# Kernel optimization log

Measured on AMD Instinct MI355X. Metric: run time of the kernel, lower is better.

The kernel has to match this reference:

```python
import jax, jax.numpy as jnp
import numpy as np

B, I, H, O, E, K = 1024, 512, 2048, 512, 8, 2


def setup_inputs() -> dict:
    key = jax.random.key(0)
    k = jax.random.split(key, 7)
    s = 0.02
    return {
        "x": jax.random.normal(k[0], (B, I), dtype=jnp.float32),
        "Wg": jax.random.normal(k[1], (I, E), dtype=jnp.float32) * s,
        "bg": jnp.zeros((E,), dtype=jnp.float32),
        "W1": jax.random.normal(k[2], (E, I, H), dtype=jnp.float32) * s,
        "b1": jnp.zeros((E, H), dtype=jnp.float32),
        "W2": jax.random.normal(k[3], (E, H, O), dtype=jnp.float32) * s,
        "b2": jnp.zeros((E, O), dtype=jnp.float32),
    }


def reference(x, Wg, bg, W1, b1, W2, b2):
    # Gating: linear -> softmax -> top-k -> renormalize (inference path,
    # no dynamic expert creation / sleep bookkeeping).
    logits = x @ Wg + bg                      # [B, E]
    probs = jax.nn.softmax(logits, axis=-1)
    top_w, top_i = jax.lax.top_k(probs, K)    # [B, K]
    top_w = top_w / jnp.sum(top_w, axis=-1, keepdims=True)
    # Dense combine weights: zero for unselected experts -> identical math to
    # the per-expert mask-gather / weighted scatter-add in the torch loop.
    combine = jnp.zeros((x.shape[0], W1.shape[0]), dtype=x.dtype)
    combine = combine.at[jnp.arange(x.shape[0])[:, None], top_i].add(top_w)  # [B, E]
    # Expert MLPs (Linear -> ReLU -> Linear), batched over experts.
    h = jax.nn.relu(jnp.einsum("bi,eih->beh", x, W1) + b1[None])  # [B, E, H]
    y = jnp.einsum("beh,eho->beo", h, W2) + b2[None]              # [B, E, O]
    out = jnp.einsum("be,beo->bo", combine, y)                    # [B, O]
    return out
```

## Files before the change

### kernel.cpp

```cpp
#include <hip/hip_runtime.h>
#include <math.h>


#define B_TOK 1024
#define I_DIM 512
#define H_DIM 2048
#define O_DIM 512
#define E_NUM 8

#define WS_COUNTS   0
#define WS_OFFSETS  32
#define WS_TOK_E    64
#define WS_TOK_W    8256
#define WS_SLOT_TOK 16448
#define WS_SLOT_WT  24640
#define WS_TOK_SLOT 32832
#define WS_XB       65536
#define WS_HB       (WS_XB + 1048576)
#define WS_Y4       (WS_HB + 8388608)

typedef __attribute__((ext_vector_type(8))) __bf16 bf16x8;
typedef __attribute__((ext_vector_type(4))) __bf16 bf16x4;
typedef __attribute__((ext_vector_type(2))) __bf16 bf16x2;
typedef __attribute__((ext_vector_type(4))) float f32x4;

#define MFMA16 __builtin_amdgcn_mfma_f32_16x16x32_bf16
#define BSTR 520

__global__ __launch_bounds__(256) void gating_kernel(
    const float* __restrict__ x, const float* __restrict__ Wg,
    const float* __restrict__ bg, __bf16* __restrict__ xb,
    int* __restrict__ tok_e, float* __restrict__ tok_w)
{
    const int lane = threadIdx.x & 63;
    const int t = blockIdx.x * 4 + (threadIdx.x >> 6);
    const float4* x4 = (const float4*)(x + (size_t)t * I_DIM);
    float4 va = x4[lane], vb = x4[lane + 64];
    bf16x4 oa, ob;
    oa[0] = (__bf16)va.x; oa[1] = (__bf16)va.y;
    oa[2] = (__bf16)va.z; oa[3] = (__bf16)va.w;
    ob[0] = (__bf16)vb.x; ob[1] = (__bf16)vb.y;
    ob[2] = (__bf16)vb.z; ob[3] = (__bf16)vb.w;
    *(bf16x4*)(xb + (size_t)t * I_DIM + lane * 4) = oa;
    *(bf16x4*)(xb + (size_t)t * I_DIM + 256 + lane * 4) = ob;

    float acc[8];
#pragma unroll
    for (int e = 0; e < 8; ++e) acc[e] = 0.f;
    float xv[8] = {va.x, va.y, va.z, va.w, vb.x, vb.y, vb.z, vb.w};
#pragma unroll
    for (int u = 0; u < 8; ++u) {
        int i = (u < 4) ? (lane * 4 + u) : (256 + lane * 4 + u - 4);
        const float4* wr = (const float4*)(Wg + (size_t)i * 8);
        float4 wa = wr[0], wb2 = wr[1];
        acc[0] = fmaf(xv[u], wa.x, acc[0]);
        acc[1] = fmaf(xv[u], wa.y, acc[1]);
        acc[2] = fmaf(xv[u], wa.z, acc[2]);
        acc[3] = fmaf(xv[u], wa.w, acc[3]);
        acc[4] = fmaf(xv[u], wb2.x, acc[4]);
        acc[5] = fmaf(xv[u], wb2.y, acc[5]);
        acc[6] = fmaf(xv[u], wb2.z, acc[6]);
        acc[7] = fmaf(xv[u], wb2.w, acc[7]);
    }
#pragma unroll
    for (int off = 32; off > 0; off >>= 1)
#pragma unroll
        for (int e = 0; e < 8; ++e)
            acc[e] += __shfl_xor(acc[e], off, 64);
    if (lane == 0) {
        float l[8];
#pragma unroll
        for (int e = 0; e < 8; ++e) l[e] = acc[e] + bg[e];
        int e0 = 0;
        for (int e = 1; e < 8; ++e) if (l[e] > l[e0]) e0 = e;
        int e1 = (e0 == 0) ? 1 : 0;
        for (int e = 0; e < 8; ++e) {
            if (e == e0) continue;
            if (l[e] > l[e1]) e1 = e;
        }
        float w0 = 1.f / (1.f + expf(l[e1] - l[e0]));
        tok_e[t * 2]     = e0;
        tok_e[t * 2 + 1] = e1;
        tok_w[t * 2]     = w0;
        tok_w[t * 2 + 1] = 1.f - w0;
    }
}

__global__ __launch_bounds__(1024) void scatter_kernel(
    const int* __restrict__ tok_e, const float* __restrict__ tok_w,
    int* __restrict__ counts, int* __restrict__ offsets,
    int* __restrict__ slot_token, float* __restrict__ slot_wt,
    int* __restrict__ tok_slot)
{
    __shared__ int hist[8], soff[8], scur[8];
    const int tid = threadIdx.x;
    if (tid < 8) { hist[tid] = 0; scur[tid] = 0; }
    __syncthreads();
    const int e0 = tok_e[tid * 2], e1 = tok_e[tid * 2 + 1];
    atomicAdd(&hist[e0], 1);
    atomicAdd(&hist[e1], 1);
    __syncthreads();
    if (tid == 0) {
        int run = 0;
        for (int e = 0; e < 8; ++e) { soff[e] = run; run += hist[e]; }
    }
    __syncthreads();
    if (tid < 8) { counts[tid] = hist[tid]; offsets[tid] = soff[tid]; }
#pragma unroll
    for (int k = 0; k < 2; ++k) {
        int e = tok_e[tid * 2 + k];
        int pos = atomicAdd(&scur[e], 1);
        int slot = soff[e] + pos;
        slot_token[slot] = tid;
        slot_wt[slot] = tok_w[tid * 2 + k];
        tok_slot[tid * 2 + k] = slot;
    }
}

template <bool IS_FC1>
__global__ __launch_bounds__(512) void moe_gemm(
    const __bf16* __restrict__ A, const float* __restrict__ Wf,
    const float* __restrict__ bias,
    const int* __restrict__ counts, const int* __restrict__ offsets,
    const int* __restrict__ slot_token,
    __bf16* __restrict__ hb, float* __restrict__ y4)
{
    constexpr int NW   = IS_FC1 ? H_DIM : O_DIM;
    constexpr int ASTR = IS_FC1 ? I_DIM : H_DIM;

    const int e  = blockIdx.z;
    const int kc = IS_FC1 ? 0 : (int)blockIdx.y;
    const int k0 = kc * 512;
    const int n0 = blockIdx.x * 64;
    const int Me = counts[e];
    if (Me == 0) return;
    const int off = offsets[e];
    const float* W = Wf + (size_t)e * (IS_FC1 ? I_DIM * H_DIM : H_DIM * O_DIM);

    __shared__ __align__(16) __bf16 Bs[64 * BSTR];

    const int tid = threadIdx.x;
    const int lane = tid & 63, w = tid >> 6;
    const int l15 = lane & 15, q = lane >> 4;

    auto stage_chunk = [&](int ch) {
        const int kb = k0 + ch * 256;
#pragma unroll
        for (int i = 0; i < 4; ++i) {
            const int u = tid + 512 * i;
            const int p = u >> 4, c4 = u & 15;
            const float* wp = W + (size_t)(kb + 2 * p) * NW + n0 + c4 * 4;
            float4 r0 = *(const float4*)wp;
            float4 r1 = *(const float4*)(wp + NW);
            const float* f0 = (const float*)&r0;
            const float* f1 = (const float*)&r1;
#pragma unroll
            for (int j = 0; j < 4; ++j) {
                bf16x2 pk;
                pk[0] = (__bf16)f0[j];
                pk[1] = (__bf16)f1[j];
                *(bf16x2*)&Bs[(size_t)(c4 * 4 + j) * BSTR + ch * 256 + 2 * p] = pk;
            }
        }
    };

    auto set_aptr = [&](int m0, const __bf16*& a0, const __bf16*& a1) {
        int mA = m0 + l15;      if (mA >= Me) mA = Me - 1;
        int mB = m0 + 16 + l15; if (mB >= Me) mB = Me - 1;
        if (IS_FC1) {
            a0 = A + (size_t)slot_token[off + mA] * ASTR + q * 8;
            a1 = A + (size_t)slot_token[off + mB] * ASTR + q * 8;
        } else {
            a0 = A + (size_t)(off + mA) * ASTR + k0 + q * 8;
            a1 = A + (size_t)(off + mB) * ASTR + k0 + q * 8;
        }
    };
    auto compute = [&](const __bf16* a0, const __bf16* a1,
                       f32x4 (&acc)[2][4], int ks0, int ks1) {
#pragma unroll 4
        for (int ks = ks0; ks < ks1; ++ks) {
            bf16x8 af0 = *(const bf16x8*)(a0 + ks * 32);
            bf16x8 af1 = *(const bf16x8*)(a1 + ks * 32);
#pragma unroll
            for (int jj = 0; jj < 4; ++jj) {
                bf16x8 bf = *(const bf16x8*)
                    &Bs[(size_t)(jj * 16 + l15) * BSTR + ks * 32 + q * 8];
                acc[0][jj] = MFMA16(af0, bf, acc[0][jj], 0, 0, 0);
                acc[1][jj] = MFMA16(af1, bf, acc[1][jj], 0, 0, 0);
            }
        }
    };
    auto epilogue = [&](int m0, f32x4 (&acc)[2][4]) {
#pragma unroll
        for (int jj = 0; jj < 4; ++jj) {
            const int gn = n0 + jj * 16 + l15;
            if (IS_FC1) {
                const float bv = bias[e * H_DIM + gn];
#pragma unroll
                for (int i = 0; i < 2; ++i)
#pragma unroll
                    for (int r = 0; r < 4; ++r) {
                        int m = m0 + i * 16 + q * 4 + r;
                        if (m < Me) {
                            float v = acc[i][jj][r] + bv;
                            hb[(size_t)(off + m) * H_DIM + gn] =
                                (__bf16)fmaxf(v, 0.f);
                        }
                    }
            } else {
#pragma unroll
                for (int i = 0; i < 2; ++i)
#pragma unroll
                    for (int r = 0; r < 4; ++r) {
                        int m = m0 + i * 16 + q * 4 + r;
                        if (m < Me)
                            y4[((size_t)kc * 2048 + off + m) * O_DIM + gn] =
                                acc[i][jj][r];
                    }
            }
        }
    };

    stage_chunk(0);
    __syncthreads();
    stage_chunk(1);

    const bool act0 = (w * 32 < Me);
    int m0 = w * 32;
    f32x4 acc[2][4] = {};
    const __bf16 *a0 = nullptr, *a1 = nullptr;
    if (act0) {
        set_aptr(m0, a0, a1);
        compute(a0, a1, acc, 0, 8);
    }
    __syncthreads();
    if (act0) {
        compute(a0, a1, acc, 8, 16);
        epilogue(m0, acc);
    }
    for (m0 = w * 32 + 256; m0 < Me; m0 += 256) {
        f32x4 acc2[2][4] = {};
        set_aptr(m0, a0, a1);
        compute(a0, a1, acc2, 0, 16);
        epilogue(m0, acc2);
    }
}

__global__ __launch_bounds__(256) void combine_kernel(
    const float* __restrict__ y4, const float* __restrict__ b2,
    const int* __restrict__ tok_slot, const int* __restrict__ tok_e,
    const float* __restrict__ tok_w, float* __restrict__ out)
{
    const int idx = blockIdx.x * 256 + threadIdx.x;
    const int t = idx >> 7;
    const int c = (idx & 127) * 4;
    float4 sum = {0.f, 0.f, 0.f, 0.f};
#pragma unroll
    for (int k = 0; k < 2; ++k) {
        const int s = tok_slot[t * 2 + k];
        const int e = tok_e[t * 2 + k];
        const float wgt = tok_w[t * 2 + k];
        float4 a = *(const float4*)(b2 + (size_t)e * O_DIM + c);
#pragma unroll
        for (int kc = 0; kc < 4; ++kc) {
            float4 v = *(const float4*)(y4 + ((size_t)kc * 2048 + s) * O_DIM + c);
            a.x += v.x; a.y += v.y; a.z += v.z; a.w += v.w;
        }
        sum.x += wgt * a.x; sum.y += wgt * a.y;
        sum.z += wgt * a.z; sum.w += wgt * a.w;
    }
    *(float4*)(out + (size_t)t * O_DIM + c) = sum;
}

extern "C" void kernel_launch(void* const* d_in, const int* in_sizes, int n_in,
                              void* d_out, int out_size, void* d_ws, size_t ws_size,
                              hipStream_t stream)
{
    const float* x  = (const float*)d_in[0];
    const float* Wg = (const float*)d_in[1];
    const float* bg = (const float*)d_in[2];
    const float* W1 = (const float*)d_in[3];
    const float* b1 = (const float*)d_in[4];
    const float* W2 = (const float*)d_in[5];
    const float* b2 = (const float*)d_in[6];
    float* out = (float*)d_out;
    char* ws = (char*)d_ws;

    int*    counts   = (int*)(ws + WS_COUNTS);
    int*    offsets  = (int*)(ws + WS_OFFSETS);
    int*    tok_e    = (int*)(ws + WS_TOK_E);
    float*  tok_w    = (float*)(ws + WS_TOK_W);
    int*    slot_tok = (int*)(ws + WS_SLOT_TOK);
    float*  slot_wt  = (float*)(ws + WS_SLOT_WT);
    int*    tok_slot = (int*)(ws + WS_TOK_SLOT);
    __bf16* xb       = (__bf16*)(ws + WS_XB);
    __bf16* hb       = (__bf16*)(ws + WS_HB);
    float*  y4       = (float*)(ws + WS_Y4);

    gating_kernel<<<B_TOK / 4, 256, 0, stream>>>(x, Wg, bg, xb, tok_e, tok_w);
    scatter_kernel<<<1, B_TOK, 0, stream>>>(tok_e, tok_w, counts, offsets,
                                            slot_tok, slot_wt, tok_slot);
    moe_gemm<true><<<dim3(32, 1, 8), 512, 0, stream>>>(
        xb, W1, b1, counts, offsets, slot_tok, hb, y4);
    moe_gemm<false><<<dim3(8, 4, 8), 512, 0, stream>>>(
        hb, W2, b2, counts, offsets, slot_tok, hb, y4);
    combine_kernel<<<(B_TOK * O_DIM / 4) / 256, 256, 0, stream>>>(
        y4, b2, tok_slot, tok_e, tok_w, out);
}
```

Baseline: 154.0 us.

## Fuse expert routing into FC1 GEMM and retile FC2 with fixed per-expert capacity

Drops the single-block scatter kernel. Each FC1 block now builds its expert's token list in shared memory with wave ballots over tok_e, and the x=0 block writes counts and tok_slot. Each expert gets fixed capacity slots, so per-expert offsets are no longer needed. FC2 now uses 32-wide N tiles and a 1024-deep K span, halving the split-K partials that combine must sum. This removes a serial launch and a pass over y partials, at the cost of redundant routing work in every FC1 block and more LDS per FC2 block.

```diff
diff --git a/kernel.cpp b/kernel.cpp
--- a/kernel.cpp
+++ b/kernel.cpp
@@ -7,17 +7,15 @@
 #define H_DIM 2048
 #define O_DIM 512
 #define E_NUM 8
+#define CAP   1024
 
 #define WS_COUNTS   0
-#define WS_OFFSETS  32
 #define WS_TOK_E    64
 #define WS_TOK_W    8256
-#define WS_SLOT_TOK 16448
-#define WS_SLOT_WT  24640
-#define WS_TOK_SLOT 32832
+#define WS_TOK_SLOT 16448
 #define WS_XB       65536
 #define WS_HB       (WS_XB + 1048576)
-#define WS_Y4       (WS_HB + 8388608)
+#define WS_Y2       (WS_HB + 33554432)
 
 typedef __attribute__((ext_vector_type(8))) __bf16 bf16x8;
 typedef __attribute__((ext_vector_type(4))) __bf16 bf16x4;
@@ -25,7 +23,6 @@
 typedef __attribute__((ext_vector_type(4))) float f32x4;
 
 #define MFMA16 __builtin_amdgcn_mfma_f32_16x16x32_bf16
-#define BSTR 520
 
 __global__ __launch_bounds__(256) void gating_kernel(
     const float* __restrict__ x, const float* __restrict__ Wg,
@@ -86,69 +83,72 @@
     }
 }
 
-__global__ __launch_bounds__(1024) void scatter_kernel(
-    const int* __restrict__ tok_e, const float* __restrict__ tok_w,
-    int* __restrict__ counts, int* __restrict__ offsets,
-    int* __restrict__ slot_token, float* __restrict__ slot_wt,
-    int* __restrict__ tok_slot)
-{
-    __shared__ int hist[8], soff[8], scur[8];
-    const int tid = threadIdx.x;
-    if (tid < 8) { hist[tid] = 0; scur[tid] = 0; }
-    __syncthreads();
-    const int e0 = tok_e[tid * 2], e1 = tok_e[tid * 2 + 1];
-    atomicAdd(&hist[e0], 1);
-    atomicAdd(&hist[e1], 1);
-    __syncthreads();
-    if (tid == 0) {
-        int run = 0;
-        for (int e = 0; e < 8; ++e) { soff[e] = run; run += hist[e]; }
-    }
-    __syncthreads();
-    if (tid < 8) { counts[tid] = hist[tid]; offsets[tid] = soff[tid]; }
-#pragma unroll
-    for (int k = 0; k < 2; ++k) {
-        int e = tok_e[tid * 2 + k];
-        int pos = atomicAdd(&scur[e], 1);
-        int slot = soff[e] + pos;
-        slot_token[slot] = tid;
-        slot_wt[slot] = tok_w[tid * 2 + k];
-        tok_slot[tid * 2 + k] = slot;
-    }
-}
-
 template <bool IS_FC1>
 __global__ __launch_bounds__(512) void moe_gemm(
     const __bf16* __restrict__ A, const float* __restrict__ Wf,
     const float* __restrict__ bias,
-    const int* __restrict__ counts, const int* __restrict__ offsets,
-    const int* __restrict__ slot_token,
-    __bf16* __restrict__ hb, float* __restrict__ y4)
+    int* __restrict__ counts, const int* __restrict__ tok_e,
+    int* __restrict__ tok_slot,
+    __bf16* __restrict__ hb, float* __restrict__ y2)
 {
-    constexpr int NW   = IS_FC1 ? H_DIM : O_DIM;
-    constexpr int ASTR = IS_FC1 ? I_DIM : H_DIM;
+    constexpr int BN    = IS_FC1 ? 64 : 32;
+    constexpr int KSPAN = IS_FC1 ? 512 : 1024;
+    constexpr int BSTR  = KSPAN + 8;
+    constexpr int NCH   = KSPAN / 256;
+    constexpr int JN    = BN / 16;
+    constexpr int C4N   = BN / 4;
+    constexpr int NW    = IS_FC1 ? H_DIM : O_DIM;
+    constexpr int ASTR  = IS_FC1 ? I_DIM : H_DIM;
 
     const int e  = blockIdx.z;
     const int kc = IS_FC1 ? 0 : (int)blockIdx.y;
-    const int k0 = kc * 512;
-    const int n0 = blockIdx.x * 64;
-    const int Me = counts[e];
-    if (Me == 0) return;
-    const int off = offsets[e];
+    const int k0 = kc * KSPAN;
+    const int n0 = blockIdx.x * BN;
+    const int off = e * CAP;
     const float* W = Wf + (size_t)e * (IS_FC1 ? I_DIM * H_DIM : H_DIM * O_DIM);
 
-    __shared__ __align__(16) __bf16 Bs[64 * BSTR];
+    __shared__ __align__(16) __bf16 Bs[BN * BSTR];
+    __shared__ int sl_tok[IS_FC1 ? CAP : 1];
+    __shared__ int sMe;
 
     const int tid = threadIdx.x;
     const int lane = tid & 63, w = tid >> 6;
     const int l15 = lane & 15, q = lane >> 4;
 
+    if (IS_FC1 && w == 0) {
+        int cnt = 0;
+#pragma unroll
+        for (int b = 0; b < 2; ++b) {
+            int vals[16];
+#pragma unroll
+            for (int c = 0; c < 16; ++c)
+                vals[c] = tok_e[(b * 16 + c) * 64 + lane];
+#pragma unroll
+            for (int c = 0; c < 16; ++c) {
+                const int gidx = (b * 16 + c) * 64 + lane;
+                const bool hit = (vals[c] == e);
+                const unsigned long long mk = __ballot(hit);
+                if (hit) {
+                    const int pos = cnt + __popcll(mk & ((1ull << lane) - 1));
+                    sl_tok[pos] = gidx >> 1;
+                    if (blockIdx.x == 0) tok_slot[gidx] = off + pos;
+                }
+                cnt += __popcll(mk);
+            }
+        }
+        if (lane == 0) {
+            sMe = cnt;
+            if (blockIdx.x == 0) counts[e] = cnt;
+        }
+    }
+    const int MeG = IS_FC1 ? 0 : counts[e];
+
     auto stage_chunk = [&](int ch) {
         const int kb = k0 + ch * 256;
 #pragma unroll
-        for (int i = 0; i < 4; ++i) {
+        for (int i = 0; i < (128 * C4N) / 512; ++i) {
             const int u = tid + 512 * i;
-            const int p = u >> 4, c4 = u & 15;
+            const int p = u / C4N, c4 = u % C4N;
             const float* wp = W + (size_t)(kb + 2 * p) * NW + n0 + c4 * 4;
             float4 r0 = *(const float4*)wp;
             float4 r1 = *(const float4*)(wp + NW);
@@ -164,25 +164,32 @@
         }
     };
 
+    stage_chunk(0);
+    __syncthreads();
+#pragma unroll
+    for (int ch = 1; ch < NCH; ++ch) stage_chunk(ch);
+
+    const int Me = IS_FC1 ? sMe : MeG;
+
     auto set_aptr = [&](int m0, const __bf16*& a0, const __bf16*& a1) {
         int mA = m0 + l15;      if (mA >= Me) mA = Me - 1;
         int mB = m0 + 16 + l15; if (mB >= Me) mB = Me - 1;
         if (IS_FC1) {
-            a0 = A + (size_t)slot_token[off + mA] * ASTR + q * 8;
-            a1 = A + (size_t)slot_token[off + mB] * ASTR + q * 8;
+            a0 = A + (size_t)sl_tok[mA] * ASTR + q * 8;
+            a1 = A + (size_t)sl_tok[mB] * ASTR + q * 8;
         } else {
             a0 = A + (size_t)(off + mA) * ASTR + k0 + q * 8;
             a1 = A + (size_t)(off + mB) * ASTR + k0 + q * 8;
         }
     };
     auto compute = [&](const __bf16* a0, const __bf16* a1,
-                       f32x4 (&acc)[2][4], int ks0, int ks1) {
+                       f32x4 (&acc)[2][JN], int ks0, int ks1) {
 #pragma unroll 4
         for (int ks = ks0; ks < ks1; ++ks) {
             bf16x8 af0 = *(const bf16x8*)(a0 + ks * 32);
             bf16x8 af1 = *(const bf16x8*)(a1 + ks * 32);
 #pragma unroll
-            for (int jj = 0; jj < 4; ++jj) {
+            for (int jj = 0; jj < JN; ++jj) {
                 bf16x8 bf = *(const bf16x8*)
                     &Bs[(size_t)(jj * 16 + l15) * BSTR + ks * 32 + q * 8];
                 acc[0][jj] = MFMA16(af0, bf, acc[0][jj], 0, 0, 0);
@@ -190,9 +197,9 @@
             }
         }
     };
-    auto epilogue = [&](int m0, f32x4 (&acc)[2][4]) {
-#pragma unroll
-        for (int jj = 0; jj < 4; ++jj) {
+    auto epilogue = [&](int m0, f32x4 (&acc)[2][JN]) {
+#pragma unroll
+        for (int jj = 0; jj < JN; ++jj) {
             const int gn = n0 + jj * 16 + l15;
             if (IS_FC1) {
                 const float bv = bias[e * H_DIM + gn];
@@ -214,20 +221,16 @@
                     for (int r = 0; r < 4; ++r) {
                         int m = m0 + i * 16 + q * 4 + r;
                         if (m < Me)
-                            y4[((size_t)kc * 2048 + off + m) * O_DIM + gn] =
+                            y2[((size_t)kc * (E_NUM * CAP) + off + m) * O_DIM + gn] =
                                 acc[i][jj][r];
                     }
             }
         }
     };
 
-    stage_chunk(0);
-    __syncthreads();
-    stage_chunk(1);
-
     const bool act0 = (w * 32 < Me);
     int m0 = w * 32;
-    f32x4 acc[2][4] = {};
+    f32x4 acc[2][JN] = {};
     const __bf16 *a0 = nullptr, *a1 = nullptr;
     if (act0) {
         set_aptr(m0, a0, a1);
@@ -235,19 +238,19 @@
     }
     __syncthreads();
     if (act0) {
-        compute(a0, a1, acc, 8, 16);
+        compute(a0, a1, acc, 8, KSPAN / 32);
         epilogue(m0, acc);
     }
     for (m0 = w * 32 + 256; m0 < Me; m0 += 256) {
-        f32x4 acc2[2][4] = {};
+        f32x4 acc2[2][JN] = {};
         set_aptr(m0, a0, a1);
-        compute(a0, a1, acc2, 0, 16);
+        compute(a0, a1, acc2, 0, KSPAN / 32);
         epilogue(m0, acc2);
     }
 }
 
 __global__ __launch_bounds__(256) void combine_kernel(
-    const float* __restrict__ y4, const float* __restrict__ b2,
+    const float* __restrict__ y2, const float* __restrict__ b2,
     const int* __restrict__ tok_slot, const int* __restrict__ tok_e,
     const float* __restrict__ tok_w, float* __restrict__ out)
 {
@@ -262,8 +265,9 @@
         const float wgt = tok_w[t * 2 + k];
         float4 a = *(const float4*)(b2 + (size_t)e * O_DIM + c);
 #pragma unroll
-        for (int kc = 0; kc < 4; ++kc) {
-            float4 v = *(const float4*)(y4 + ((size_t)kc * 2048 + s) * O_DIM + c);
+        for (int kc = 0; kc < 2; ++kc) {
+            float4 v = *(const float4*)
+                (y2 + ((size_t)kc * (E_NUM * CAP) + s) * O_DIM + c);
             a.x += v.x; a.y += v.y; a.z += v.z; a.w += v.w;
         }
         sum.x += wgt * a.x; sum.y += wgt * a.y;
@@ -287,23 +291,18 @@
     char* ws = (char*)d_ws;
 
     int*    counts   = (int*)(ws + WS_COUNTS);
-    int*    offsets  = (int*)(ws + WS_OFFSETS);
     int*    tok_e    = (int*)(ws + WS_TOK_E);
     float*  tok_w    = (float*)(ws + WS_TOK_W);
-    int*    slot_tok = (int*)(ws + WS_SLOT_TOK);
-    float*  slot_wt  = (float*)(ws + WS_SLOT_WT);
     int*    tok_slot = (int*)(ws + WS_TOK_SLOT);
     __bf16* xb       = (__bf16*)(ws + WS_XB);
     __bf16* hb       = (__bf16*)(ws + WS_HB);
-    float*  y4       = (float*)(ws + WS_Y4);
+    float*  y2       = (float*)(ws + WS_Y2);
 
     gating_kernel<<<B_TOK / 4, 256, 0, stream>>>(x, Wg, bg, xb, tok_e, tok_w);
-    scatter_kernel<<<1, B_TOK, 0, stream>>>(tok_e, tok_w, counts, offsets,
-                                            slot_tok, slot_wt, tok_slot);
     moe_gemm<true><<<dim3(32, 1, 8), 512, 0, stream>>>(
-        xb, W1, b1, counts, offsets, slot_tok, hb, y4);
-    moe_gemm<false><<<dim3(8, 4, 8), 512, 0, stream>>>(
-        hb, W2, b2, counts, offsets, slot_tok, hb, y4);
+        xb, W1, b1, counts, tok_e, tok_slot, hb, y2);
+    moe_gemm<false><<<dim3(16, 2, 8), 512, 0, stream>>>(
+        hb, W2, b2, counts, tok_e, tok_slot, hb, y2);
     combine_kernel<<<(B_TOK * O_DIM / 4) / 256, 256, 0, stream>>>(
-        y4, b2, tok_slot, tok_e, tok_w, out);
+        y2, b2, tok_slot, tok_e, tok_w, out);
 }
```

After: 155.7 us. Within noise of the previous version (+1.1%).
